# Kernel tuning notes

Measured on AMD Instinct MI355X. Metric: run time of the kernel, lower is better.

Reference implementation:

```python
import jax, jax.numpy as jnp
import numpy as np

FLTRSTDEV = 2.0
EXTGRADFAC = 10.0
DMAX = 15.0
ENHANCEMENT = 2.0   # enhancement_factor in the module
NEG_WEIGHT = 1.5    # negative_weight in the module


def make_gauss_edge_fltr(stdev: float) -> np.ndarray:
    """Gaussian-derivative edge filter, shape [2, 1, k, k] (OIHW), k = 2*ceil(2*stdev)+1."""
    r = int(np.ceil(2.0 * stdev))
    x = np.arange(-r, r + 1, dtype=np.float32)
    g = np.exp(-x ** 2 / (2.0 * stdev ** 2)).astype(np.float32)
    g /= g.sum()
    dg = (-x / (stdev ** 2)) * np.exp(-x ** 2 / (2.0 * stdev ** 2))
    dg = (dg / np.abs(dg).sum()).astype(np.float32)
    f_dy = np.outer(dg, g)   # gradient along axis 0
    f_dx = np.outer(g, dg)   # gradient along axis 1
    return np.stack([f_dy, f_dx])[:, None]  # [2,1,k,k]


def cmpt_grad_im(img, fltr):
    """img: [B,1,H,W], fltr: [2,1,k,k] -> [B,2,H,W] gradient image (SAME conv)."""
    return jax.lax.conv_general_dilated(
        img, fltr, window_strides=(1, 1), padding='SAME',
        dimension_numbers=('NCHW', 'OIHW', 'NCHW'))


def setup_inputs() -> dict:
    key = jax.random.key(0)
    k1, k2 = jax.random.split(key)
    B, H, W = 16, 1024, 1024
    # predicted signed distance map, roughly in [-DMAX, DMAX]
    pred_dmap = jax.random.normal(k1, (B, 1, H, W), dtype=jnp.float32) * 5.0
    # stand-in for the snake-rendered signed distance map (detached target)
    snake_dm = jax.random.normal(k2, (B, 1, H, W), dtype=jnp.float32) * 5.0
    fltr = jnp.asarray(make_gauss_edge_fltr(FLTRSTDEV))
    return {"pred_dmap": pred_dmap, "snake_dm": snake_dm, "fltr": fltr}


def reference(pred_dmap, snake_dm, fltr):
    # external-energy gradient images driving the snakes
    gimg = cmpt_grad_im(pred_dmap, fltr) * EXTGRADFAC           # [B,2,H,W]
    gimgW = cmpt_grad_im(jnp.abs(pred_dmap), fltr) * EXTGRADFAC  # [B,2,H,W]
    # dmap[dmap > 0] = dmax  (background set to +dmax)
    sd = jnp.where(snake_dm > 0, DMAX, snake_dm)
    # snake_dm[snake_dm < 0] *= enhancement_factor
    sd = jnp.where(sd < 0, sd * ENHANCEMENT, sd)
    neg_mask = (sd < 0).astype(pred_dmap.dtype)
    squared_diff = (pred_dmap - jax.lax.stop_gradient(sd)) ** 2
    loss = jnp.mean(squared_diff * (1.0 + neg_mask * NEG_WEIGHT))
    return loss, gimg, gimgW
```

## Files before the change

kernel.cpp:

```cpp
#include <hip/hip_runtime.h>

#define HH 1024
#define WW 1024
#define BB 16
#define ROWS 32
#define DMAXC 15.0f
#define ENHC 2.0f
#define NEGWC 1.5f
#define EGFC 10.0f

__device__ __forceinline__ float lossterm(float p, float s) {
    float sd = (s > 0.f) ? DMAXC : s;
    sd = (sd < 0.f) ? sd * ENHC : sd;
    float w = (sd < 0.f) ? (1.f + NEGWC) : 1.f;
    float d = p - sd;
    return d * d * w;
}

__device__ __forceinline__ float rfl(float x) {
    return __uint_as_float(__builtin_amdgcn_readfirstlane(__float_as_uint(x)));
}

#define HROW(SLOT, J, DOLOSS)                                                 \
    {                                                                         \
        const int yin_ = r0 - 4 + (J);                                        \
        if (lane < 18) {                                                      \
            const int gc_ = c0 - 4 + 4 * lane;                                \
            float4 v4_ = make_float4(0.f, 0.f, 0.f, 0.f);                     \
            if ((unsigned)yin_ < HH && (unsigned)gc_ < WW)                    \
                v4_ = *(const float4*)&img[(size_t)yin_ * WW + gc_];          \
            *(float4*)&s_row[wid][4 * lane] = v4_;                            \
        }                                                                     \
        asm volatile("s_waitcnt lgkmcnt(0)" ::: "memory");                    \
        float sv_ = 0.f;                                                      \
        if (DOLOSS) sv_ = snk[(size_t)yin_ * WW + c0 + lane];                 \
        float hg_ = 0.f, hd_ = 0.f, ag_ = 0.f, ad_ = 0.f, pv_ = 0.f;          \
        _Pragma("unroll")                                                     \
        for (int k_ = 0; k_ < 9; ++k_) {                                      \
            float v_ = s_row[wid][lane + k_];                                 \
            if (k_ == 4) pv_ = v_;                                            \
            float a_ = fabsf(v_);               \
            hg_ += g[k_] * v_;                                                \
            hd_ += dg[k_] * v_;                                               \
            ag_ += g[k_] * a_;                                                \
            ad_ += dg[k_] * a_;                                               \
        }                                                                     \
        hgP[SLOT] = hg_; hdP[SLOT] = hd_;                                     \
        hgA[SLOT] = ag_; hdA[SLOT] = ad_;                                     \
        if (DOLOSS) lsum += lossterm(pv_, sv_);                               \
    }

#define EMIT(YO, BASE)                                                        \
    {                                                                         \
        float c0_ = 0.f, c1_ = 0.f, w0_ = 0.f, w1_ = 0.f;                     \
        _Pragma("unroll")                                                     \
        for (int i_ = 0; i_ < 9; ++i_) {                                      \
            const int s_ = ((BASE) + i_) % 9;               \
            c0_ += dgE[i_] * hgP[s_];                                         \
            c1_ += gE[i_] * hdP[s_];                                          \
            w0_ += dgE[i_] * hgA[s_];                                         \
            w1_ += gE[i_] * hdA[s_];                                          \
        }                                                                     \
        const size_t o_ = (size_t)(YO) * WW + c0 + lane;                      \
        g0[o_] = c0_;                                                         \
        g1[o_] = c1_;                                                         \
        g0W[o_] = w0_;                                                        \
        g1W[o_] = w1_;                                                        \
    }

__global__ __launch_bounds__(256) void snake_rows(
    const float* __restrict__ pred, const float* __restrict__ snake,
    const float* __restrict__ fltr, float* __restrict__ out)
{
    __shared__ float s_row[4][72];
    __shared__ float s_red[4];

    const int t = threadIdx.x;
    const int lane = t & 63;
    const int wid = t >> 6;
    const int b = blockIdx.z;
    const int r0 = blockIdx.y * ROWS;
    const int c0 = blockIdx.x * 256 + wid * 64;

    float g[9], dg[9], gE[9], dgE[9];
#pragma unroll
    for (int i = 0; i < 9; ++i) {
        float s = 0.f;
#pragma unroll
        for (int j = 0; j < 9; ++j) s += fltr[i * 9 + j];
        dg[i] = rfl(s);
        dgE[i] = rfl(EGFC * s);
    }
    {
        float inv = 1.f / dg[0];
#pragma unroll
        for (int j = 0; j < 9; ++j) {
            g[j] = rfl(fltr[j] * inv);
            gE[j] = rfl(EGFC * g[j]);
        }
    }

    const float* img = pred + (size_t)b * (HH * WW);
    const float* snk = snake + (size_t)b * (HH * WW);
    float* g0 = out + 1 + ((size_t)(b * 2 + 0)) * (HH * WW);
    float* g1 = out + 1 + ((size_t)(b * 2 + 1)) * (HH * WW);
    float* g0W = g0 + (size_t)BB * 2 * HH * WW;
    float* g1W = g1 + (size_t)BB * 2 * HH * WW;

    float hgP[9], hdP[9], hgA[9], hdA[9];
    float lsum = 0.f;

#pragma unroll
    for (int u = 0; u < 9; ++u) { HROW(u, u, (u >= 4)); }
    EMIT(r0, 0);

#pragma unroll 1
    for (int m = 0; m < 3; ++m) {
        const int jb = 9 + 9 * m;
#pragma unroll
        for (int u = 0; u < 9; ++u) {
            HROW(u, jb + u, true);
            EMIT(r0 + jb + u - 8, (u + 1) % 9);
        }
    }

#pragma unroll
    for (int u = 0; u < 4; ++u) {
        HROW(u, 36 + u, false);
        EMIT(r0 + 28 + u, (u + 1) % 9);
    }

#pragma unroll
    for (int off = 32; off > 0; off >>= 1) lsum += __shfl_down(lsum, off);
    if (lane == 0) s_red[wid] = lsum;
    __syncthreads();
    if (t == 0) {
        float tot = s_red[0] + s_red[1] + s_red[2] + s_red[3];
        atomicAdd(out, tot * (1.0f / 16777216.0f));
    }
}

extern "C" void kernel_launch(void* const* d_in, const int* in_sizes, int n_in,
                              void* d_out, int out_size, void* d_ws, size_t ws_size,
                              hipStream_t stream) {
    const float* pred = (const float*)d_in[0];
    const float* snake = (const float*)d_in[1];
    const float* fltr = (const float*)d_in[2];
    float* out = (float*)d_out;

    hipMemsetAsync(out, 0, sizeof(float), stream);

    dim3 grid(WW / 256, HH / ROWS, BB);
    snake_rows<<<grid, 256, 0, stream>>>(pred, snake, fltr, out);
}
```

Before: 414.5 us.

## Prefetch 9-row input chunks into registers while computing the previous chunk

Replaces the per-row load-then-wait pattern with chunked software pipelining. Each wave prefetches the next 9 input rows into registers as float4 loads spread across 54 lanes, and loads the snake values for the chunk up front. It computes the current chunk from a 9-row LDS buffer, then writes the prefetched rows into LDS. The aim is to hide global load latency behind the convolution math, at the cost of more registers and LDS per block, which may lower occupancy.

```diff
diff --git a/kernel.cpp b/kernel.cpp
--- a/kernel.cpp
+++ b/kernel.cpp
@@ -21,23 +21,37 @@
     return __uint_as_float(__builtin_amdgcn_readfirstlane(__float_as_uint(x)));
 }
 
-#define HROW(SLOT, J, DOLOSS)                                                 \
+#define PRELOAD(JB, NR)                                                       \
     {                                                                         \
-        const int yin_ = r0 - 4 + (J);                                        \
-        if (lane < 18) {                                                      \
-            const int gc_ = c0 - 4 + 4 * lane;                                \
-            float4 v4_ = make_float4(0.f, 0.f, 0.f, 0.f);                     \
-            if ((unsigned)yin_ < HH && (unsigned)gc_ < WW)                    \
-                v4_ = *(const float4*)&img[(size_t)yin_ * WW + gc_];          \
-            *(float4*)&s_row[wid][4 * lane] = v4_;                            \
+        pA = pB = pC = make_float4(0.f, 0.f, 0.f, 0.f);                       \
+        const int gc_ = c0 - 4 + 4 * lpos;                                    \
+        if (lane < 54 && (unsigned)gc_ < WW) {                                \
+            const int y0_ = r0 - 4 + (JB) + lrow;                             \
+            if (lrow < (NR) && (unsigned)y0_ < HH)                            \
+                pA = *(const float4*)&img[(size_t)y0_ * WW + gc_];            \
+            if (3 + lrow < (NR) && (unsigned)(y0_ + 3) < HH)                  \
+                pB = *(const float4*)&img[(size_t)(y0_ + 3) * WW + gc_];      \
+            if (6 + lrow < (NR) && (unsigned)(y0_ + 6) < HH)                  \
+                pC = *(const float4*)&img[(size_t)(y0_ + 6) * WW + gc_];      \
+        }                                                                     \
+    }
+
+#define WRITECHUNK(NR)                                                        \
+    {                                                                         \
+        if (lane < 54) {                                                      \
+            if (lrow < (NR))     *(float4*)&s_ch[wid][lrow][4 * lpos] = pA;   \
+            if (3 + lrow < (NR)) *(float4*)&s_ch[wid][3 + lrow][4 * lpos] = pB;\
+            if (6 + lrow < (NR)) *(float4*)&s_ch[wid][6 + lrow][4 * lpos] = pC;\
         }                                                                     \
         asm volatile("s_waitcnt lgkmcnt(0)" ::: "memory");                    \
-        float sv_ = 0.f;                                                      \
-        if (DOLOSS) sv_ = snk[(size_t)yin_ * WW + c0 + lane];                 \
+    }
+
+#define CROW(SLOT, U, DOLOSS)                                                 \
+    {                                                                         \
         float hg_ = 0.f, hd_ = 0.f, ag_ = 0.f, ad_ = 0.f, pv_ = 0.f;          \
         _Pragma("unroll")                                                     \
         for (int k_ = 0; k_ < 9; ++k_) {                                      \
-            float v_ = s_row[wid][lane + k_];                                 \
+            float v_ = s_ch[wid][U][lane + k_];                               \
             if (k_ == 4) pv_ = v_;                                            \
             float a_ = fabsf(v_);               \
             hg_ += g[k_] * v_;                                                \
@@ -47,7 +61,7 @@
         }                                                                     \
         hgP[SLOT] = hg_; hdP[SLOT] = hd_;                                     \
         hgA[SLOT] = ag_; hdA[SLOT] = ad_;                                     \
-        if (DOLOSS) lsum += lossterm(pv_, sv_);                               \
+        if (DOLOSS) lsum += lossterm(pv_, svv[U]);                            \
     }
 
 #define EMIT(YO, BASE)                                                        \
@@ -72,12 +86,14 @@
     const float* __restrict__ pred, const float* __restrict__ snake,
     const float* __restrict__ fltr, float* __restrict__ out)
 {
-    __shared__ float s_row[4][72];
+    __shared__ float s_ch[4][9][72];
     __shared__ float s_red[4];
 
     const int t = threadIdx.x;
     const int lane = t & 63;
     const int wid = t >> 6;
+    const int lrow = lane / 18;
+    const int lpos = lane - 18 * lrow;
     const int b = blockIdx.z;
     const int r0 = blockIdx.y * ROWS;
     const int c0 = blockIdx.x * 256 + wid * 64;
@@ -108,25 +124,43 @@
     float* g1W = g1 + (size_t)BB * 2 * HH * WW;
 
     float hgP[9], hdP[9], hgA[9], hdA[9];
+    float svv[9];
+    float4 pA, pB, pC;
     float lsum = 0.f;
 
+    PRELOAD(0, 9);
+    WRITECHUNK(9);
+
+    PRELOAD(9, 9);
 #pragma unroll
-    for (int u = 0; u < 9; ++u) { HROW(u, u, (u >= 4)); }
+    for (int u = 4; u < 9; ++u)
+        svv[u] = snk[(size_t)(r0 - 4 + u) * WW + c0 + lane];
+#pragma unroll
+    for (int u = 0; u < 9; ++u) { CROW(u, u, (u >= 4)); }
     EMIT(r0, 0);
+    asm volatile("" ::: "memory");
+    WRITECHUNK(9);
 
 #pragma unroll 1
     for (int m = 0; m < 3; ++m) {
         const int jb = 9 + 9 * m;
+        const int nrn = (m == 2) ? 4 : 9;
+        PRELOAD(jb + 9, nrn);
+#pragma unroll
+        for (int u = 0; u < 9; ++u)
+            svv[u] = snk[(size_t)(r0 - 4 + jb + u) * WW + c0 + lane];
 #pragma unroll
         for (int u = 0; u < 9; ++u) {
-            HROW(u, jb + u, true);
+            CROW(u, u, true);
             EMIT(r0 + jb + u - 8, (u + 1) % 9);
         }
+        asm volatile("" ::: "memory");
+        WRITECHUNK(nrn);
     }
 
 #pragma unroll
     for (int u = 0; u < 4; ++u) {
-        HROW(u, 36 + u, false);
+        CROW(u, u, false);
         EMIT(r0 + 28 + u, (u + 1) % 9);
     }
 
```

New measurement: 390.0 us. -5.9%, faster.
